# Optimization experiments

Hardware: AMD Instinct MI355X
Metric: run time of the kernel (lower is better)

## Reference

```python
import jax, jax.numpy as jnp
import numpy as np

D_MODEL = 1024
NUM_HEADS = 16
DEPTH = D_MODEL // NUM_HEADS


def setup_inputs() -> dict:
    key = jax.random.key(0)
    ks = jax.random.split(key, 6)
    B, S = 2, 2048
    scale = 1.0 / np.sqrt(D_MODEL)
    return {
        "q": jax.random.normal(ks[0], (B, S, D_MODEL), jnp.float32),
        "k": jax.random.normal(ks[1], (B, S, D_MODEL), jnp.float32),
        "v": jax.random.normal(ks[2], (B, S, D_MODEL), jnp.float32),
        "wq": jax.random.normal(ks[3], (D_MODEL, D_MODEL), jnp.float32) * scale,
        "wk": jax.random.normal(ks[4], (D_MODEL, D_MODEL), jnp.float32) * scale,
        "wv": jax.random.normal(ks[5], (D_MODEL, D_MODEL), jnp.float32) * scale,
    }


def reference(q, k, v, wq, wk, wv):
    B, S, _ = q.shape
    # Linear projections (nn.Linear: x @ W.T), then split heads -> [B,H,S,depth]
    def split(x):
        return x.reshape(B, -1, NUM_HEADS, DEPTH).transpose(0, 2, 1, 3)
    Q = split(q @ wq.T)
    K = split(k @ wk.T)
    V = split(v @ wv.T)
    scores = jnp.einsum("bhqd,bhkd->bhqk", Q, K) / np.sqrt(DEPTH).astype(np.float32)
    attn = jax.nn.softmax(scores, axis=-1)
    out = jnp.einsum("bhqk,bhkd->bhqd", attn, V)
    # merge heads; note: original forward never applies self.dense
    return out.transpose(0, 2, 1, 3).reshape(B, S, D_MODEL)
```

## Files before the change

kernel.cpp:

```cpp
#include <hip/hip_runtime.h>
#include <hip/hip_bf16.h>
#include <stdint.h>

#define B_SZ 2
#define S_LEN 2048
#define DM 1024
#define NH 16
#define DEPTH 64
#define M_ROWS (B_SZ * S_LEN)
#define SCALE_Q 0.1803368801111144f

typedef __attribute__((ext_vector_type(8))) short bf16x8;
typedef __attribute__((ext_vector_type(4))) float f32x4;
typedef __attribute__((ext_vector_type(16))) float f32x16;

__device__ __forceinline__ unsigned short f2bf(float x) {
    union { float f; unsigned u; } a; a.f = x;
    unsigned r = a.u + 0x7FFF + ((a.u >> 16) & 1);
    return (unsigned short)(r >> 16);
}

__device__ __forceinline__ bf16x8 u4_to_bf8(uint4 u) {
    union { uint4 a; bf16x8 b; } c; c.a = u; return c.b;
}

__device__ __forceinline__ unsigned cvtpk_bf16(float lo, float hi) {
    unsigned r;
    asm("v_cvt_pk_bf16_f32 %0, %1, %2" : "=v"(r) : "v"(lo), "v"(hi));
    return r;
}

__device__ __forceinline__ void permswap32(unsigned &a, unsigned &b) {
    auto r = __builtin_amdgcn_permlane32_swap(a, b, false, false);
    a = r[0]; b = r[1];
}

__device__ __forceinline__ void async_ld16(const unsigned short* g, void* l) {
    __builtin_amdgcn_global_load_lds(
        (const __attribute__((address_space(1))) void*)g,
        (__attribute__((address_space(3))) void*)l,
        16, 0, 0);
}


__global__ __launch_bounds__(256)
void convert_kernel(const float* __restrict__ q, const float* __restrict__ k,
                    const float* __restrict__ v, const float* __restrict__ wq,
                    const float* __restrict__ wk, const float* __restrict__ wv,
                    unsigned short* __restrict__ dst) {
    const int z = blockIdx.y;
    const float* src = (z == 0) ? q : (z == 1) ? k : (z == 2) ? v
                     : (z == 3) ? wq : (z == 4) ? wk : wv;
    const size_t n4  = (z < 3) ? ((size_t)M_ROWS * DM / 4) : ((size_t)DM * DM / 4);
    const size_t off = (z < 3) ? ((size_t)z * M_ROWS * DM)
                               : ((size_t)3 * M_ROWS * DM + (size_t)(z - 3) * DM * DM);
    unsigned short* d = dst + off;
    const size_t stride = (size_t)gridDim.x * blockDim.x;
    for (size_t i = (size_t)blockIdx.x * blockDim.x + threadIdx.x; i < n4; i += stride) {
        float4 x = ((const float4*)src)[i];
        ushort4 p;
        p.x = f2bf(x.x); p.y = f2bf(x.y); p.z = f2bf(x.z); p.w = f2bf(x.w);
        ((ushort4*)d)[i] = p;
    }
}

__global__ __launch_bounds__(256)
void proj_gemm3_kernel(const unsigned short* __restrict__ Xall,
                       const unsigned short* __restrict__ Wall,
                       unsigned short* __restrict__ Call) {
    __shared__ unsigned short As[128 * 64];
    __shared__ unsigned short Bs[128 * 64];

    const int z = blockIdx.z;
    const unsigned short* X = Xall + (size_t)z * M_ROWS * DM;
    const unsigned short* W = Wall + (size_t)z * DM * DM;
    unsigned short* C = Call + (size_t)z * M_ROWS * DM;

    const int tid  = threadIdx.x;
    const int wave = tid >> 6;
    const int lane = tid & 63;
    const int l32  = lane & 31;
    const int s    = lane >> 5;
    const int m0 = blockIdx.x * 128;
    const int n0 = blockIdx.y * 128;
    const int wm = (wave >> 1) * 64;
    const int wn = (wave & 1) * 64;

    const int r8 = lane >> 3;
    const int sc = (lane & 7) ^ r8;

    f32x16 acc[2][2];
#pragma unroll
    for (int mi = 0; mi < 2; ++mi)
#pragma unroll
        for (int ni = 0; ni < 2; ++ni)
#pragma unroll
            for (int r = 0; r < 16; ++r) acc[mi][ni][r] = 0.f;

    for (int k0 = 0; k0 < DM; k0 += 64) {
#pragma unroll
        for (int i = 0; i < 4; ++i) {
            const int r = i * 32 + wave * 8 + r8;
            async_ld16(X + (size_t)(m0 + r) * DM + k0 + sc * 8,
                       (char*)As + i * 4096 + wave * 1024);
            async_ld16(W + (size_t)(n0 + r) * DM + k0 + sc * 8,
                       (char*)Bs + i * 4096 + wave * 1024);
        }
        __syncthreads();

#pragma unroll
        for (int ch = 0; ch < 4; ++ch) {
            bf16x8 af[2], bfr[2];
#pragma unroll
            for (int mi = 0; mi < 2; ++mi) {
                const int row = wm + mi * 32 + l32;
                af[mi] = *(const bf16x8*)&As[row * 64 + (((2 * ch + s) ^ (row & 7)) * 8)];
            }
#pragma unroll
            for (int ni = 0; ni < 2; ++ni) {
                const int row = wn + ni * 32 + l32;
                bfr[ni] = *(const bf16x8*)&Bs[row * 64 + (((2 * ch + s) ^ (row & 7)) * 8)];
            }
#pragma unroll
            for (int mi = 0; mi < 2; ++mi)
#pragma unroll
                for (int ni = 0; ni < 2; ++ni)
                    acc[mi][ni] = __builtin_amdgcn_mfma_f32_32x32x16_bf16(
                        af[mi], bfr[ni], acc[mi][ni], 0, 0, 0);
        }
        __syncthreads();
    }

    const float scale = (z == 0) ? SCALE_Q : 1.0f;
#pragma unroll
    for (int mi = 0; mi < 2; ++mi)
#pragma unroll
        for (int ni = 0; ni < 2; ++ni)
#pragma unroll
            for (int r = 0; r < 16; ++r) {
                const int row = m0 + wm + mi * 32 + (r & 3) + 8 * (r >> 2) + 4 * s;
                const int col = n0 + wn + ni * 32 + l32;
                C[(size_t)row * DM + col] = f2bf(acc[mi][ni][r] * scale);
            }
}

__global__ __launch_bounds__(256)
void vtrans_kernel(const unsigned short* __restrict__ Vp,
                   unsigned short* __restrict__ Vt) {
    __shared__ unsigned short Ls[64 * 72];
    const int tr = blockIdx.x;
    const int h  = blockIdx.y;
    const int tid = threadIdx.x;

#pragma unroll
    for (int i = 0; i < 2; ++i) {
        const int id = i * 256 + tid;
        const int r = id >> 3, c = id & 7;
        bf16x8 v8 = *(const bf16x8*)&Vp[(size_t)(tr * 64 + r) * DM + h * 64 + c * 8];
        *(bf16x8*)&Ls[r * 72 + ((c ^ (r & 7)) * 8)] = v8;
    }
    __syncthreads();

    const int b = tr >> 5;
    const int col0 = (tr & 31) * 64;
#pragma unroll
    for (int i = 0; i < 2; ++i) {
        const int id = i * 256 + tid;
        const int d = id >> 3, c2 = id & 7;
        unsigned short tmp[8];
#pragma unroll
        for (int j = 0; j < 8; ++j) {
            const int t = c2 * 8 + j;
            tmp[j] = Ls[t * 72 + (((d >> 3) ^ (t & 7)) * 8) + (d & 7)];
        }
        *(bf16x8*)&Vt[(size_t)((b * NH + h) * DEPTH + d) * S_LEN + col0 + c2 * 8] =
            *(const bf16x8*)tmp;
    }
}

__global__ __launch_bounds__(128, 2)
void attn8_kernel(const unsigned short* __restrict__ Qp,
                  const unsigned short* __restrict__ Kp,
                  const unsigned short* __restrict__ Vt,
                  float* __restrict__ out,
                  float* __restrict__ Op1,
                  float* __restrict__ lp) {
    __shared__ __align__(16) char smem[34816];
    unsigned short* Ks = (unsigned short*)smem;
    unsigned short* Vs = (unsigned short*)(smem + 8192);
    unsigned int*   Ps = (unsigned int*)(smem + 24576);

    const int tid  = threadIdx.x;
    const int w    = tid >> 6;
    const int lane = tid & 63;
    const int l32  = lane & 31;
    const int s    = lane >> 5;
    const int r8   = lane >> 3;
    const int sc   = (lane & 7) ^ r8;

    const int q0 = blockIdx.x * 128 + w * 64;
    const int h  = blockIdx.y;
    const int z  = blockIdx.z;
    const int b     = z >> 1;
    const int split = z & 1;
    const int tbase = split * 1024;

    const unsigned short* Kg = Kp + (size_t)(b * S_LEN + tbase) * DM + h * DEPTH;
    const unsigned short* Vg = Vt + (size_t)((b * NH + h) * DEPTH) * S_LEN + tbase;
    float* obase = split ? Op1 : out;
    float* lbase = lp + (size_t)split * M_ROWS * NH;
    unsigned int* PsW = Ps + w * 1280;

    bf16x8 qf[2][4];
#pragma unroll
    for (int nq = 0; nq < 2; ++nq) {
        const unsigned short* p =
            Qp + (size_t)(b * S_LEN + q0 + nq * 32 + l32) * DM + h * DEPTH;
#pragma unroll
        for (int ch = 0; ch < 4; ++ch)
            qf[nq][ch] = *(const bf16x8*)(p + ch * 16 + s * 8);
    }

    f32x16 oacc[2][2];
    float lacc[2] = {0.f, 0.f};
#pragma unroll
    for (int db = 0; db < 2; ++db)
#pragma unroll
        for (int nq = 0; nq < 2; ++nq)
#pragma unroll
            for (int r = 0; r < 16; ++r) oacc[db][nq][r] = 0.f;

#pragma unroll
    for (int i = 0; i < 2; ++i)
        async_ld16(Kg + (size_t)(w * 16 + i * 8 + r8) * DM + sc * 8,
                   (char*)Ks + w * 2048 + i * 1024);
#pragma unroll
    for (int i = 0; i < 4; ++i)
        async_ld16(Vg + (size_t)(w * 32 + i * 8 + r8) * S_LEN + sc * 8,
                   (char*)Vs + w * 4096 + i * 1024);

    for (int it = 0; it < 32; ++it) {
        const int kb = it & 1;
        const int vb = (it >> 1) & 1;

        asm volatile("s_waitcnt vmcnt(0) lgkmcnt(0)" ::: "memory");
        __syncthreads();

        if (it < 31) {
            const int tk = (it + 1) * 32;
            char* kd = (char*)Ks + (kb ^ 1) * 4096 + w * 2048;
#pragma unroll
            for (int i = 0; i < 2; ++i)
                async_ld16(Kg + (size_t)(tk + w * 16 + i * 8 + r8) * DM + sc * 8,
                           kd + i * 1024);
        }
        if (!(it & 1) && it < 30) {
            const int tv = ((it >> 1) + 1) * 64;
            char* vd = (char*)Vs + (vb ^ 1) * 8192 + w * 4096;
#pragma unroll
            for (int i = 0; i < 4; ++i)
                async_ld16(Vg + (size_t)(w * 32 + i * 8 + r8) * S_LEN + tv + sc * 8,
                           vd + i * 1024);
        }

        const unsigned short* Kb = Ks + kb * 2048;
        const unsigned short* Vb = Vs + vb * 4096;
        const int vcb = (it & 1) * 4;

        f32x16 s0, s1;
#pragma unroll
        for (int r = 0; r < 16; ++r) { s0[r] = 0.f; s1[r] = 0.f; }
#pragma unroll
        for (int ch = 0; ch < 4; ++ch) {
            bf16x8 kf = *(const bf16x8*)
                &Kb[l32 * 64 + (((2 * ch + s) ^ (l32 & 7)) * 8)];
            s0 = __builtin_amdgcn_mfma_f32_32x32x16_bf16(kf, qf[0][ch], s0, 0, 0, 0);
            s1 = __builtin_amdgcn_mfma_f32_32x32x16_bf16(kf, qf[1][ch], s1, 0, 0, 0);
        }

        unsigned pw[2][8];
#pragma unroll
        for (int nq = 0; nq < 2; ++nq) {
            float p[16];
#pragma unroll
            for (int r = 0; r < 16; ++r)
                p[r] = __builtin_amdgcn_exp2f(nq ? s1[r] : s0[r]);
            lacc[nq] += ((p[0] + p[1]) + (p[2] + p[3]))
                      + ((p[4] + p[5]) + (p[6] + p[7]))
                      + ((p[8] + p[9]) + (p[10] + p[11]))
                      + ((p[12] + p[13]) + (p[14] + p[15]));
            unsigned a0 = cvtpk_bf16(p[0],  p[1]);
            unsigned b0 = cvtpk_bf16(p[4],  p[5]);
            unsigned a1 = cvtpk_bf16(p[2],  p[3]);
            unsigned b1 = cvtpk_bf16(p[6],  p[7]);
            unsigned a2 = cvtpk_bf16(p[8],  p[9]);
            unsigned b2 = cvtpk_bf16(p[12], p[13]);
            unsigned a3 = cvtpk_bf16(p[10], p[11]);
            unsigned b3 = cvtpk_bf16(p[14], p[15]);
            permswap32(a0, b0);
            permswap32(a1, b1);
            permswap32(a2, b2);
            permswap32(a3, b3);
            pw[nq][0] = a0; pw[nq][1] = a1; pw[nq][2] = b0; pw[nq][3] = b1;
            pw[nq][4] = a2; pw[nq][5] = a3; pw[nq][6] = b2; pw[nq][7] = b3;
        }

#pragma unroll
        for (int ch = 0; ch < 2; ++ch) {
            bf16x8 pf[2];
#pragma unroll
            for (int nq = 0; nq < 2; ++nq) {
                uint4 pu;
                pu.x = pw[nq][ch * 4 + 0];
                pu.y = pw[nq][ch * 4 + 1];
                pu.z = pw[nq][ch * 4 + 2];
                pu.w = pw[nq][ch * 4 + 3];
                pf[nq] = u4_to_bf8(pu);
            }
#pragma unroll
            for (int db = 0; db < 2; ++db) {
                const int drow = db * 32 + l32;
                bf16x8 vf = *(const bf16x8*)
                    &Vb[drow * 64 + (((vcb + 2 * ch + s) ^ (drow & 7)) * 8)];
                oacc[db][0] = __builtin_amdgcn_mfma_f32_32x32x16_bf16(
                    vf, pf[0], oacc[db][0], 0, 0, 0);
                oacc[db][1] = __builtin_amdgcn_mfma_f32_32x32x16_bf16(
                    vf, pf[1], oacc[db][1], 0, 0, 0);
            }
        }
    }

    asm volatile("s_waitcnt vmcnt(0)" ::: "memory");

    const float l0 = lacc[0] + __shfl_xor(lacc[0], 32, 64);
    const float l1 = lacc[1] + __shfl_xor(lacc[1], 32, 64);
    if (s == 0) {
        lbase[(size_t)(b * S_LEN + q0 + l32) * NH + h]      = l0;
        lbase[(size_t)(b * S_LEN + q0 + 32 + l32) * NH + h] = l1;
    }

    asm volatile("" ::: "memory");
    float* Of = (float*)PsW;
#pragma unroll
    for (int c = 0; c < 4; ++c) {
        const int nq = c >> 1;
        if ((l32 >> 4) == (c & 1)) {
            const int qh = l32 & 15;
#pragma unroll
            for (int db = 0; db < 2; ++db)
#pragma unroll
                for (int m = 0; m < 4; ++m) {
                    float4 v;
                    v.x = oacc[db][nq][4 * m + 0];
                    v.y = oacc[db][nq][4 * m + 1];
                    v.z = oacc[db][nq][4 * m + 2];
                    v.w = oacc[db][nq][4 * m + 3];
                    *(float4*)&Of[qh * 68 + db * 32 + 8 * m + 4 * s] = v;
                }
        }
        asm volatile("" ::: "memory");
#pragma unroll
        for (int i = 0; i < 4; ++i) {
            const int row = i * 4 + (lane >> 4);
            const int c4 = lane & 15;
            float4 v = *(const float4*)&Of[row * 68 + c4 * 4];
            *(float4*)&obase[(size_t)(b * S_LEN + q0 + c * 16 + row) * DM
                             + h * DEPTH + c4 * 4] = v;
        }
        asm volatile("" ::: "memory");
    }
}

__global__ __launch_bounds__(256)
void combine_kernel(float* __restrict__ out, const float* __restrict__ Op1,
                    const float* __restrict__ lp) {
    const int i4 = blockIdx.x * 256 + threadIdx.x;
    const int row = i4 >> 8;
    const int c4  = i4 & 255;
    const int h   = c4 >> 4;
    const float l = lp[row * NH + h] + lp[M_ROWS * NH + row * NH + h];
    const float inv = 1.0f / l;
    float4 a = ((const float4*)out)[i4];
    float4 bq = ((const float4*)Op1)[i4];
    a.x = (a.x + bq.x) * inv;
    a.y = (a.y + bq.y) * inv;
    a.z = (a.z + bq.z) * inv;
    a.w = (a.w + bq.w) * inv;
    ((float4*)out)[i4] = a;
}

#define LDK 72

__global__ __launch_bounds__(256)
void proj_gemm_kernel(const float* __restrict__ q, const float* __restrict__ k,
                      const float* __restrict__ v, const float* __restrict__ wq,
                      const float* __restrict__ wk, const float* __restrict__ wv,
                      unsigned short* __restrict__ Qp, unsigned short* __restrict__ Kp,
                      unsigned short* __restrict__ Vp) {
    __shared__ unsigned short As[128 * LDK];
    __shared__ unsigned short Bs[128 * LDK];

    const int z = blockIdx.z;
    const float* __restrict__ X = (z == 0) ? q : (z == 1) ? k : v;
    const float* __restrict__ W = (z == 0) ? wq : (z == 1) ? wk : wv;
    unsigned short* __restrict__ C = (z == 0) ? Qp : (z == 1) ? Kp : Vp;

    const int tid  = threadIdx.x;
    const int wave = tid >> 6;
    const int lane = tid & 63;
    const int quad = lane >> 4;
    const int l16  = lane & 15;
    const int m0 = blockIdx.x * 128;
    const int n0 = blockIdx.y * 128;
    const int wm = (wave >> 1) * 64;
    const int wn = (wave & 1) * 64;

    f32x4 acc[4][4];
#pragma unroll
    for (int mt = 0; mt < 4; ++mt)
#pragma unroll
        for (int nt = 0; nt < 4; ++nt)
            acc[mt][nt] = (f32x4){0.f, 0.f, 0.f, 0.f};

    for (int k0 = 0; k0 < DM; k0 += 64) {
#pragma unroll
        for (int vv = 0; vv < 8; ++vv) {
            int vecid = tid + 256 * vv;
            int r  = vecid >> 4;
            int c4 = vecid & 15;
            const float4 xa = *(const float4*)&X[(size_t)(m0 + r) * DM + k0 + c4 * 4];
            ushort4 pa;
            pa.x = f2bf(xa.x); pa.y = f2bf(xa.y); pa.z = f2bf(xa.z); pa.w = f2bf(xa.w);
            *(ushort4*)&As[r * LDK + c4 * 4] = pa;
            const float4 xb = *(const float4*)&W[(size_t)(n0 + r) * DM + k0 + c4 * 4];
            ushort4 pb;
            pb.x = f2bf(xb.x); pb.y = f2bf(xb.y); pb.z = f2bf(xb.z); pb.w = f2bf(xb.w);
            *(ushort4*)&Bs[r * LDK + c4 * 4] = pb;
        }
        __syncthreads();

#pragma unroll
        for (int kc = 0; kc < 2; ++kc) {
            bf16x8 af[4], bfr[4];
#pragma unroll
            for (int mt = 0; mt < 4; ++mt)
                af[mt] = *(const bf16x8*)&As[(wm + mt * 16 + l16) * LDK + kc * 32 + quad * 8];
#pragma unroll
            for (int nt = 0; nt < 4; ++nt)
                bfr[nt] = *(const bf16x8*)&Bs[(wn + nt * 16 + l16) * LDK + kc * 32 + quad * 8];
#pragma unroll
            for (int mt = 0; mt < 4; ++mt)
#pragma unroll
                for (int nt = 0; nt < 4; ++nt)
                    acc[mt][nt] = __builtin_amdgcn_mfma_f32_16x16x32_bf16(
                        af[mt], bfr[nt], acc[mt][nt], 0, 0, 0);
        }
        __syncthreads();
    }

#pragma unroll
    for (int mt = 0; mt < 4; ++mt)
#pragma unroll
        for (int nt = 0; nt < 4; ++nt)
#pragma unroll
            for (int r = 0; r < 4; ++r) {
                int row = m0 + wm + mt * 16 + quad * 4 + r;
                int col = n0 + wn + nt * 16 + l16;
                C[(size_t)row * DM + col] = f2bf(acc[mt][nt][r]);
            }
}

__global__ __launch_bounds__(256)
void attn_kernel(const unsigned short* __restrict__ Qp,
                 const unsigned short* __restrict__ Kp,
                 const unsigned short* __restrict__ Vp,
                 float* __restrict__ out) {
    __shared__ unsigned short Ks[64 * LDK];
    __shared__ unsigned short Vtl[64 * LDK];
    __shared__ unsigned short Ps[4 * 16 * LDK];

    const int tid  = threadIdx.x;
    const int wave = tid >> 6;
    const int lane = tid & 63;
    const int quad = lane >> 4;
    const int l16  = lane & 15;
    const int q0 = blockIdx.x * 64;
    const int h  = blockIdx.y;
    const int b  = blockIdx.z;
    const int wbase = wave * 16 * LDK;

    bf16x8 qf[2];
    {
        size_t row = (size_t)b * S_LEN + q0 + wave * 16 + l16;
        const unsigned short* p = Qp + row * DM + h * DEPTH;
        qf[0] = *(const bf16x8*)(p + quad * 8);
        qf[1] = *(const bf16x8*)(p + 32 + quad * 8);
    }

    float m_i[4], l_i[4];
    f32x4 accO[4];
#pragma unroll
    for (int r = 0; r < 4; ++r) { m_i[r] = -1e30f; l_i[r] = 0.f; }
#pragma unroll
    for (int f = 0; f < 4; ++f) accO[f] = (f32x4){0.f, 0.f, 0.f, 0.f};

    for (int t0 = 0; t0 < S_LEN; t0 += 64) {
#pragma unroll
        for (int vv = 0; vv < 2; ++vv) {
            int vecid = tid + 256 * vv;
            int r  = vecid >> 3;
            int cv = vecid & 7;
            size_t grow = (size_t)(b * S_LEN + t0 + r) * DM + h * DEPTH + cv * 8;
            *(bf16x8*)&Ks[r * LDK + cv * 8] = *(const bf16x8*)(Kp + grow);
            bf16x8 vvv = *(const bf16x8*)(Vp + grow);
#pragma unroll
            for (int j = 0; j < 8; ++j)
                Vtl[(cv * 8 + j) * LDK + r] = ((const unsigned short*)&vvv)[j];
        }
        __syncthreads();

        f32x4 sc4[4];
#pragma unroll
        for (int nt = 0; nt < 4; ++nt) {
            f32x4 a = (f32x4){0.f, 0.f, 0.f, 0.f};
            bf16x8 kf0 = *(const bf16x8*)&Ks[(nt * 16 + l16) * LDK + quad * 8];
            bf16x8 kf1 = *(const bf16x8*)&Ks[(nt * 16 + l16) * LDK + 32 + quad * 8];
            a = __builtin_amdgcn_mfma_f32_16x16x32_bf16(qf[0], kf0, a, 0, 0, 0);
            a = __builtin_amdgcn_mfma_f32_16x16x32_bf16(qf[1], kf1, a, 0, 0, 0);
            sc4[nt] = a;
        }
#pragma unroll
        for (int nt = 0; nt < 4; ++nt)
#pragma unroll
            for (int r = 0; r < 4; ++r) sc4[nt][r] *= 0.125f;

#pragma unroll
        for (int r = 0; r < 4; ++r) {
            float mx = fmaxf(fmaxf(sc4[0][r], sc4[1][r]), fmaxf(sc4[2][r], sc4[3][r]));
#pragma unroll
            for (int off = 1; off < 16; off <<= 1)
                mx = fmaxf(mx, __shfl_xor(mx, off, 64));
            float mnew = fmaxf(m_i[r], mx);
            float alpha = __expf(m_i[r] - mnew);
            float rs = 0.f;
#pragma unroll
            for (int nt = 0; nt < 4; ++nt) {
                float p = __expf(sc4[nt][r] - mnew);
                sc4[nt][r] = p;
                rs += p;
            }
#pragma unroll
            for (int off = 1; off < 16; off <<= 1)
                rs += __shfl_xor(rs, off, 64);
            l_i[r] = l_i[r] * alpha + rs;
            m_i[r] = mnew;
#pragma unroll
            for (int f = 0; f < 4; ++f) accO[f][r] *= alpha;
        }

#pragma unroll
        for (int nt = 0; nt < 4; ++nt)
#pragma unroll
            for (int r = 0; r < 4; ++r)
                Ps[wbase + (quad * 4 + r) * LDK + nt * 16 + l16] = f2bf(sc4[nt][r]);
        __syncthreads();

        bf16x8 pf0 = *(const bf16x8*)&Ps[wbase + l16 * LDK + quad * 8];
        bf16x8 pf1 = *(const bf16x8*)&Ps[wbase + l16 * LDK + 32 + quad * 8];
#pragma unroll
        for (int f = 0; f < 4; ++f) {
            bf16x8 vf0 = *(const bf16x8*)&Vtl[(f * 16 + l16) * LDK + quad * 8];
            bf16x8 vf1 = *(const bf16x8*)&Vtl[(f * 16 + l16) * LDK + 32 + quad * 8];
            accO[f] = __builtin_amdgcn_mfma_f32_16x16x32_bf16(pf0, vf0, accO[f], 0, 0, 0);
            accO[f] = __builtin_amdgcn_mfma_f32_16x16x32_bf16(pf1, vf1, accO[f], 0, 0, 0);
        }
        __syncthreads();
    }

#pragma unroll
    for (int f = 0; f < 4; ++f)
#pragma unroll
        for (int r = 0; r < 4; ++r) {
            size_t row = (size_t)b * S_LEN + q0 + wave * 16 + quad * 4 + r;
            out[row * DM + h * DEPTH + f * 16 + l16] = accO[f][r] / l_i[r];
        }
}

extern "C" void kernel_launch(void* const* d_in, const int* in_sizes, int n_in,
                              void* d_out, int out_size, void* d_ws, size_t ws_size,
                              hipStream_t stream) {
    const float* q  = (const float*)d_in[0];
    const float* k  = (const float*)d_in[1];
    const float* v  = (const float*)d_in[2];
    const float* wq = (const float*)d_in[3];
    const float* wk = (const float*)d_in[4];
    const float* wv = (const float*)d_in[5];
    float* out = (float*)d_out;

    unsigned short* ws = (unsigned short*)d_ws;
    const size_t NPROJ = (size_t)M_ROWS * DM;
    const size_t NW    = (size_t)DM * DM;

    const size_t need = (3 * NPROJ + 3 * NW + 3 * NPROJ) * sizeof(unsigned short);

    if (ws_size >= need) {
        unsigned short* Xbf = ws;
        unsigned short* Wbf = ws + 3 * NPROJ;
        unsigned short* Cp  = ws + 3 * NPROJ + 3 * NW;
        unsigned short* Qp  = Cp;
        unsigned short* Kp  = Cp + NPROJ;
        unsigned short* Vp  = Cp + 2 * NPROJ;
        unsigned short* Vt  = ws;
        float*          Op1 = (float*)(ws + NPROJ);
        float*          lp  = (float*)(ws + 3 * NPROJ);

        convert_kernel<<<dim3(256, 6), 256, 0, stream>>>(q, k, v, wq, wk, wv, Xbf);
        proj_gemm3_kernel<<<dim3(M_ROWS / 128, DM / 128, 3), 256, 0, stream>>>(Xbf, Wbf, Cp);
        vtrans_kernel<<<dim3(M_ROWS / 64, NH), 256, 0, stream>>>(Vp, Vt);
        attn8_kernel<<<dim3(S_LEN / 128, NH, 4), 128, 0, stream>>>(
            Qp, Kp, Vt, out, Op1, lp);
        combine_kernel<<<dim3(M_ROWS * DM / 4 / 256), 256, 0, stream>>>(out, Op1, lp);
    } else {
        unsigned short* Qp = ws;
        unsigned short* Kp = ws + NPROJ;
        unsigned short* Vp = ws + 2 * NPROJ;
        proj_gemm_kernel<<<dim3(M_ROWS / 128, DM / 128, 3), 256, 0, stream>>>(
            q, k, v, wq, wk, wv, Qp, Kp, Vp);
        attn_kernel<<<dim3(S_LEN / 64, NH, B_SZ), 256, 0, stream>>>(Qp, Kp, Vp, out);
    }
}
```

Measured before the change: 190.6 us.

## Load K and V in 64-key tiles per iteration, halving barriers, and add MFMA priority hints

```diff
diff --git a/kernel.cpp b/kernel.cpp
--- a/kernel.cpp
+++ b/kernel.cpp
@@ -185,10 +185,9 @@
                   float* __restrict__ out,
                   float* __restrict__ Op1,
                   float* __restrict__ lp) {
-    __shared__ __align__(16) char smem[34816];
+    __shared__ __align__(16) char smem[32768];
     unsigned short* Ks = (unsigned short*)smem;
-    unsigned short* Vs = (unsigned short*)(smem + 8192);
-    unsigned int*   Ps = (unsigned int*)(smem + 24576);
+    unsigned short* Vs = (unsigned short*)(smem + 16384);
 
     const int tid  = threadIdx.x;
     const int w    = tid >> 6;
@@ -209,7 +208,6 @@
     const unsigned short* Vg = Vt + (size_t)((b * NH + h) * DEPTH) * S_LEN + tbase;
     float* obase = split ? Op1 : out;
     float* lbase = lp + (size_t)split * M_ROWS * NH;
-    unsigned int* PsW = Ps + w * 1280;
 
     bf16x8 qf[2][4];
 #pragma unroll
@@ -231,101 +229,106 @@
             for (int r = 0; r < 16; ++r) oacc[db][nq][r] = 0.f;
 
 #pragma unroll
-    for (int i = 0; i < 2; ++i)
-        async_ld16(Kg + (size_t)(w * 16 + i * 8 + r8) * DM + sc * 8,
-                   (char*)Ks + w * 2048 + i * 1024);
+    for (int i = 0; i < 4; ++i)
+        async_ld16(Kg + (size_t)(w * 32 + i * 8 + r8) * DM + sc * 8,
+                   (char*)smem + w * 4096 + i * 1024);
 #pragma unroll
     for (int i = 0; i < 4; ++i)
         async_ld16(Vg + (size_t)(w * 32 + i * 8 + r8) * S_LEN + sc * 8,
-                   (char*)Vs + w * 4096 + i * 1024);
-
-    for (int it = 0; it < 32; ++it) {
-        const int kb = it & 1;
-        const int vb = (it >> 1) & 1;
+                   (char*)smem + 16384 + w * 4096 + i * 1024);
+
+    for (int it = 0; it < 16; ++it) {
+        const int cb = it & 1;
 
         asm volatile("s_waitcnt vmcnt(0) lgkmcnt(0)" ::: "memory");
         __syncthreads();
 
-        if (it < 31) {
-            const int tk = (it + 1) * 32;
-            char* kd = (char*)Ks + (kb ^ 1) * 4096 + w * 2048;
-#pragma unroll
-            for (int i = 0; i < 2; ++i)
-                async_ld16(Kg + (size_t)(tk + w * 16 + i * 8 + r8) * DM + sc * 8,
+        if (it < 15) {
+            const int tn = (it + 1) * 64;
+            char* kd = (char*)smem + (cb ^ 1) * 8192 + w * 4096;
+            char* vd = (char*)smem + 16384 + (cb ^ 1) * 8192 + w * 4096;
+#pragma unroll
+            for (int i = 0; i < 4; ++i)
+                async_ld16(Kg + (size_t)(tn + w * 32 + i * 8 + r8) * DM + sc * 8,
                            kd + i * 1024);
-        }
-        if (!(it & 1) && it < 30) {
-            const int tv = ((it >> 1) + 1) * 64;
-            char* vd = (char*)Vs + (vb ^ 1) * 8192 + w * 4096;
 #pragma unroll
             for (int i = 0; i < 4; ++i)
-                async_ld16(Vg + (size_t)(w * 32 + i * 8 + r8) * S_LEN + tv + sc * 8,
+                async_ld16(Vg + (size_t)(w * 32 + i * 8 + r8) * S_LEN + tn + sc * 8,
                            vd + i * 1024);
         }
 
-        const unsigned short* Kb = Ks + kb * 2048;
-        const unsigned short* Vb = Vs + vb * 4096;
-        const int vcb = (it & 1) * 4;
-
-        f32x16 s0, s1;
-#pragma unroll
-        for (int r = 0; r < 16; ++r) { s0[r] = 0.f; s1[r] = 0.f; }
-#pragma unroll
-        for (int ch = 0; ch < 4; ++ch) {
-            bf16x8 kf = *(const bf16x8*)
-                &Kb[l32 * 64 + (((2 * ch + s) ^ (l32 & 7)) * 8)];
-            s0 = __builtin_amdgcn_mfma_f32_32x32x16_bf16(kf, qf[0][ch], s0, 0, 0, 0);
-            s1 = __builtin_amdgcn_mfma_f32_32x32x16_bf16(kf, qf[1][ch], s1, 0, 0, 0);
-        }
-
-        unsigned pw[2][8];
-#pragma unroll
-        for (int nq = 0; nq < 2; ++nq) {
-            float p[16];
-#pragma unroll
-            for (int r = 0; r < 16; ++r)
-                p[r] = __builtin_amdgcn_exp2f(nq ? s1[r] : s0[r]);
-            lacc[nq] += ((p[0] + p[1]) + (p[2] + p[3]))
-                      + ((p[4] + p[5]) + (p[6] + p[7]))
-                      + ((p[8] + p[9]) + (p[10] + p[11]))
-                      + ((p[12] + p[13]) + (p[14] + p[15]));
-            unsigned a0 = cvtpk_bf16(p[0],  p[1]);
-            unsigned b0 = cvtpk_bf16(p[4],  p[5]);
-            unsigned a1 = cvtpk_bf16(p[2],  p[3]);
-            unsigned b1 = cvtpk_bf16(p[6],  p[7]);
-            unsigned a2 = cvtpk_bf16(p[8],  p[9]);
-            unsigned b2 = cvtpk_bf16(p[12], p[13]);
-            unsigned a3 = cvtpk_bf16(p[10], p[11]);
-            unsigned b3 = cvtpk_bf16(p[14], p[15]);
-            permswap32(a0, b0);
-            permswap32(a1, b1);
-            permswap32(a2, b2);
-            permswap32(a3, b3);
-            pw[nq][0] = a0; pw[nq][1] = a1; pw[nq][2] = b0; pw[nq][3] = b1;
-            pw[nq][4] = a2; pw[nq][5] = a3; pw[nq][6] = b2; pw[nq][7] = b3;
-        }
-
-#pragma unroll
-        for (int ch = 0; ch < 2; ++ch) {
-            bf16x8 pf[2];
+        const unsigned short* Kb = Ks + cb * 4096;
+        const unsigned short* Vb = Vs + cb * 4096;
+
+#pragma unroll
+        for (int th = 0; th < 2; ++th) {
+            const unsigned short* Kh = Kb + th * 2048;
+            const int vcb = th * 4;
+
+            f32x16 s0, s1;
+#pragma unroll
+            for (int r = 0; r < 16; ++r) { s0[r] = 0.f; s1[r] = 0.f; }
+            __builtin_amdgcn_s_setprio(1);
+#pragma unroll
+            for (int ch = 0; ch < 4; ++ch) {
+                bf16x8 kf = *(const bf16x8*)
+                    &Kh[l32 * 64 + (((2 * ch + s) ^ (l32 & 7)) * 8)];
+                s0 = __builtin_amdgcn_mfma_f32_32x32x16_bf16(kf, qf[0][ch], s0, 0, 0, 0);
+                s1 = __builtin_amdgcn_mfma_f32_32x32x16_bf16(kf, qf[1][ch], s1, 0, 0, 0);
+            }
+            __builtin_amdgcn_s_setprio(0);
+
+            unsigned pw[2][8];
 #pragma unroll
             for (int nq = 0; nq < 2; ++nq) {
-                uint4 pu;
-                pu.x = pw[nq][ch * 4 + 0];
-                pu.y = pw[nq][ch * 4 + 1];
-                pu.z = pw[nq][ch * 4 + 2];
-                pu.w = pw[nq][ch * 4 + 3];
-                pf[nq] = u4_to_bf8(pu);
-            }
-#pragma unroll
-            for (int db = 0; db < 2; ++db) {
-                const int drow = db * 32 + l32;
-                bf16x8 vf = *(const bf16x8*)
-                    &Vb[drow * 64 + (((vcb + 2 * ch + s) ^ (drow & 7)) * 8)];
-                oacc[db][0] = __builtin_amdgcn_mfma_f32_32x32x16_bf16(
-                    vf, pf[0], oacc[db][0], 0, 0, 0);
-                oacc[db][1] = __builtin_amdgcn_mfma_f32_32x32x16_bf16(
-                    vf, pf[1], oacc[db][1], 0, 0, 0);
+                float p[16];
+#pragma unroll
+                for (int r = 0; r < 16; ++r)
+                    p[r] = __builtin_amdgcn_exp2f(nq ? s1[r] : s0[r]);
+                lacc[nq] += ((p[0] + p[1]) + (p[2] + p[3]))
+                          + ((p[4] + p[5]) + (p[6] + p[7]))
+                          + ((p[8] + p[9]) + (p[10] + p[11]))
+                          + ((p[12] + p[13]) + (p[14] + p[15]));
+                unsigned a0 = cvtpk_bf16(p[0],  p[1]);
+                unsigned b0 = cvtpk_bf16(p[4],  p[5]);
+                unsigned a1 = cvtpk_bf16(p[2],  p[3]);
+                unsigned b1 = cvtpk_bf16(p[6],  p[7]);
+                unsigned a2 = cvtpk_bf16(p[8],  p[9]);
+                unsigned b2 = cvtpk_bf16(p[12], p[13]);
+                unsigned a3 = cvtpk_bf16(p[10], p[11]);
+                unsigned b3 = cvtpk_bf16(p[14], p[15]);
+                permswap32(a0, b0);
+                permswap32(a1, b1);
+                permswap32(a2, b2);
+                permswap32(a3, b3);
+                pw[nq][0] = a0; pw[nq][1] = a1; pw[nq][2] = b0; pw[nq][3] = b1;
+                pw[nq][4] = a2; pw[nq][5] = a3; pw[nq][6] = b2; pw[nq][7] = b3;
+            }
+
+#pragma unroll
+            for (int ch = 0; ch < 2; ++ch) {
+                bf16x8 pf[2];
+#pragma unroll
+                for (int nq = 0; nq < 2; ++nq) {
+                    uint4 pu;
+                    pu.x = pw[nq][ch * 4 + 0];
+                    pu.y = pw[nq][ch * 4 + 1];
+                    pu.z = pw[nq][ch * 4 + 2];
+                    pu.w = pw[nq][ch * 4 + 3];
+                    pf[nq] = u4_to_bf8(pu);
+                }
+                __builtin_amdgcn_s_setprio(1);
+#pragma unroll
+                for (int db = 0; db < 2; ++db) {
+                    const int drow = db * 32 + l32;
+                    bf16x8 vf = *(const bf16x8*)
+                        &Vb[drow * 64 + (((vcb + 2 * ch + s) ^ (l32 & 7)) * 8)];
+                    oacc[db][0] = __builtin_amdgcn_mfma_f32_32x32x16_bf16(
+                        vf, pf[0], oacc[db][0], 0, 0, 0);
+                    oacc[db][1] = __builtin_amdgcn_mfma_f32_32x32x16_bf16(
+                        vf, pf[1], oacc[db][1], 0, 0, 0);
+                }
+                __builtin_amdgcn_s_setprio(0);
             }
         }
     }
@@ -339,8 +342,8 @@
         lbase[(size_t)(b * S_LEN + q0 + 32 + l32) * NH + h] = l1;
     }
 
-    asm volatile("" ::: "memory");
-    float* Of = (float*)PsW;
+    __syncthreads();
+    float* Of = (float*)(smem + w * 4608);
 #pragma unroll
     for (int c = 0; c < 4; ++c) {
         const int nq = c >> 1;
```

Result: slower. 198.1 us (+3.9%).
